# Performance work log

Measured on AMD Instinct MI355X. Metric: run time of the kernel, lower is better.

The kernel has to match this reference:

```python
import jax, jax.numpy as jnp
import numpy as np

DIM = 512
HEADS = 8
LANDMARKS = 64


def setup_inputs() -> dict:
    key = jax.random.key(0)
    ks = jax.random.split(key, 9)
    B, N, C = 2, 16384, DIM
    s = 0.02
    return {
        "x": jax.random.normal(ks[0], (B, N, C), dtype=jnp.float32),
        "wq": jax.random.normal(ks[1], (C, C), dtype=jnp.float32) * s,
        "bq": jnp.zeros((C,), dtype=jnp.float32),
        "wk": jax.random.normal(ks[2], (C, C), dtype=jnp.float32) * s,
        "bk": jnp.zeros((C,), dtype=jnp.float32),
        "wv": jax.random.normal(ks[3], (C, C), dtype=jnp.float32) * s,
        "bv": jnp.zeros((C,), dtype=jnp.float32),
        "wo": jax.random.normal(ks[4], (C, C), dtype=jnp.float32) * s,
        "bo": jnp.zeros((C,), dtype=jnp.float32),
    }


def _to_heads(x, H):
    B, N, C = x.shape
    return x.reshape(B, N, H, C // H).transpose(0, 2, 1, 3)  # (B,H,N,hd)


def reference(x, wq, bq, wk, bk, wv, bv, wo, bo):
    B, N, C = x.shape
    H = HEADS
    hd = C // H
    scale = hd ** (-0.5)
    m = min(LANDMARKS, N)

    q = _to_heads(x @ wq.T + bq, H) * scale  # (B,H,N,hd)
    k = _to_heads(x @ wk.T + bk, H)
    v = _to_heads(x @ wv.T + bv, H)

    if N <= m * 2:
        attn = jax.nn.softmax(jnp.einsum("bhnd,bhkd->bhnk", q, k), axis=-1)
        out = jnp.einsum("bhnk,bhkd->bhnd", attn, v)
    else:
        seg = (N + m - 1) // m
        pad = seg * m - N
        if pad > 0:
            q_p = jnp.pad(q, ((0, 0), (0, 0), (0, pad), (0, 0)))
            k_p = jnp.pad(k, ((0, 0), (0, 0), (0, pad), (0, 0)))
        else:
            q_p, k_p = q, k
        # landmarks: mean over consecutive segments of length seg (zero-pad included, as in torch)
        q_land = q_p.reshape(B, H, m, seg, hd).mean(3)  # (B,H,m,hd)
        k_land = k_p.reshape(B, H, m, seg, hd).mean(3)

        ker1 = jax.nn.softmax(jnp.einsum("bhnd,bhmd->bhnm", q, k_land), axis=-1)  # (B,H,N,m)
        ker2 = jax.nn.softmax(jnp.einsum("bhld,bhmd->bhlm", q_land, k_land), axis=-1)  # (B,H,m,m)
        ker3 = jax.nn.softmax(jnp.einsum("bhmd,bhnd->bhmn", q_land, k), axis=-1)  # (B,H,m,N)
        ker2_inv = jnp.linalg.pinv(ker2)  # (B,H,m,m)

        kv = jnp.einsum("bhmn,bhnd->bhmd", ker3, v)  # (B,H,m,hd)
        out = jnp.einsum("bhnm,bhmd->bhnd", ker1, ker2_inv @ kv)

    out = out.transpose(0, 2, 1, 3).reshape(B, N, C)
    return out @ wo.T + bo
```

## Files before the change

kernel.cpp:

```cpp
#include <hip/hip_runtime.h>
#include <stdint.h>


constexpr int B_   = 2;
constexpr int N_   = 16384;
constexpr int C_   = 512;
constexpr int H_   = 8;
constexpr int HD_  = 64;
constexpr int LM_  = 64;
constexpr int SEG_ = 256;
constexpr int BH_  = 16;
constexpr int NCH_ = 16;
constexpr int NPART_ = 64;
constexpr int SW1_ = 3;
constexpr int SW2_ = 2;

#define RCOND_ (640.0 * 1.1920928955078125e-07)

typedef unsigned short ushort4_t __attribute__((ext_vector_type(4)));
typedef unsigned short ushort8_t __attribute__((ext_vector_type(8)));
typedef __bf16 bf16x8 __attribute__((ext_vector_type(8)));
typedef float f32x4 __attribute__((ext_vector_type(4)));

__device__ inline float bf2f(unsigned short u) {
  union { unsigned int i; float f; } x; x.i = ((unsigned int)u) << 16; return x.f;
}
__device__ inline unsigned short f2bf(float f) {
  union { float f; unsigned int i; } x; x.f = f;
  unsigned int lsb = (x.i >> 16) & 1;
  return (unsigned short)((x.i + 0x7fffu + lsb) >> 16);
}
__device__ inline bf16x8 ld_bf8(const unsigned short* p) { return *(const bf16x8*)p; }

__device__ __forceinline__ void gload_lds16(const unsigned short* gsrc, unsigned short* ldst) {
  __builtin_amdgcn_global_load_lds((const __attribute__((address_space(1))) void*)gsrc,
                                   (__attribute__((address_space(3))) void*)ldst, 16, 0, 0);
}

__global__ __launch_bounds__(256) void cvt_w4_kernel(const float* __restrict__ wq,
                                                     const float* __restrict__ wk,
                                                     const float* __restrict__ wv,
                                                     const float* __restrict__ wo,
                                                     unsigned short* __restrict__ dq,
                                                     unsigned short* __restrict__ dk,
                                                     unsigned short* __restrict__ dv,
                                                     unsigned short* __restrict__ dwo) {
  int which = blockIdx.y;
  const float* src = which == 0 ? wq : which == 1 ? wk : which == 2 ? wv : wo;
  unsigned short* dst = which == 0 ? dq : which == 1 ? dk : which == 2 ? dv : dwo;
  int i = blockIdx.x * 256 + threadIdx.x;
  const float* s = src + (size_t)i * 8;
  float4 x0 = *(const float4*)(s);
  float4 x1 = *(const float4*)(s + 4);
  ushort8_t u;
  u[0] = f2bf(x0.x); u[1] = f2bf(x0.y); u[2] = f2bf(x0.z); u[3] = f2bf(x0.w);
  u[4] = f2bf(x1.x); u[5] = f2bf(x1.y); u[6] = f2bf(x1.z); u[7] = f2bf(x1.w);
  *(ushort8_t*)(dst + (size_t)i * 8) = u;
}

__global__ __launch_bounds__(256) void seg_mean_kernel(const float* __restrict__ x,
                                                       float* __restrict__ xbar,
                                                       unsigned short* __restrict__ xb) {
  int bl = blockIdx.x;
  int b = bl / LM_, l = bl % LM_;
  int t = threadIdx.x;
  int c4 = t & 127;
  int rh = t >> 7;
  const size_t rowbase = (size_t)b * N_ + (size_t)l * SEG_;
  const float* xp = x + rowbase * C_;
  float4 s = make_float4(0.f, 0.f, 0.f, 0.f);
  for (int r = rh * 128; r < rh * 128 + 128; ++r) {
    float4 v = *(const float4*)(xp + (size_t)r * C_ + c4 * 4);
    s.x += v.x; s.y += v.y; s.z += v.z; s.w += v.w;
    ushort4_t u;
    u[0] = f2bf(v.x); u[1] = f2bf(v.y); u[2] = f2bf(v.z); u[3] = f2bf(v.w);
    *(ushort4_t*)(xb + (rowbase + r) * C_ + c4 * 4) = u;
  }
  __shared__ float red[2][512];
  *(float4*)&red[rh][c4 * 4] = s;
  __syncthreads();
  if (rh == 0) {
    float4 a = *(float4*)&red[0][c4 * 4];
    float4 c = *(float4*)&red[1][c4 * 4];
    const float invs = 1.0f / SEG_;
    float4 o;
    o.x = (a.x + c.x) * invs; o.y = (a.y + c.y) * invs;
    o.z = (a.z + c.z) * invs; o.w = (a.w + c.w) * invs;
    *(float4*)(xbar + (size_t)bl * C_ + c4 * 4) = o;
  }
}

__global__ __launch_bounds__(256) void land_gemm_kernel(const float* __restrict__ xbar,
                                                        const float* __restrict__ wq,
                                                        const float* __restrict__ bq,
                                                        const float* __restrict__ wk,
                                                        const float* __restrict__ bk,
                                                        float* __restrict__ qland,
                                                        float* __restrict__ kland,
                                                        unsigned short* __restrict__ qlbh,
                                                        unsigned short* __restrict__ qlbl,
                                                        unsigned short* __restrict__ klb) {
  __shared__ float As[32][68];
  __shared__ float Ws[32][68];
  int which = blockIdx.x >> 1;
  int row0 = (blockIdx.x & 1) * 64;
  int col0 = blockIdx.y * 64;
  const float* A = xbar;
  const float* W = which ? wk : wq;
  const float* bias = which ? bk : bq;
  float scale = which ? 1.0f : 0.125f;
  float* out = which ? kland : qland;
  int tid = threadIdx.x;
  int tm = tid >> 4, tn = tid & 15;
  float acc[4][4] = {};
  for (int k0 = 0; k0 < C_; k0 += 32) {
#pragma unroll
    for (int i = 0; i < 2; ++i) {
      int s = tid + i * 256;
      int r = s >> 3;
      int kg = (s & 7) << 2;
      float4 av = *(const float4*)(A + (size_t)(row0 + r) * C_ + k0 + kg);
      As[kg + 0][r] = av.x; As[kg + 1][r] = av.y;
      As[kg + 2][r] = av.z; As[kg + 3][r] = av.w;
      float4 wv = *(const float4*)(W + (size_t)(col0 + r) * C_ + k0 + kg);
      Ws[kg + 0][r] = wv.x; Ws[kg + 1][r] = wv.y;
      Ws[kg + 2][r] = wv.z; Ws[kg + 3][r] = wv.w;
    }
    __syncthreads();
#pragma unroll
    for (int kk = 0; kk < 32; ++kk) {
      float4 a = *(const float4*)&As[kk][tm * 4];
      float4 b = *(const float4*)&Ws[kk][tn * 4];
      float av[4] = {a.x, a.y, a.z, a.w};
      float bv[4] = {b.x, b.y, b.z, b.w};
#pragma unroll
      for (int i = 0; i < 4; ++i)
#pragma unroll
        for (int j = 0; j < 4; ++j) acc[i][j] += av[i] * bv[j];
    }
    __syncthreads();
  }
#pragma unroll
  for (int i = 0; i < 4; ++i) {
    int row = row0 + tm * 4 + i;
    int d0 = tn * 4;
    float o4[4];
#pragma unroll
    for (int j = 0; j < 4; ++j) o4[j] = (acc[i][j] + bias[col0 + d0 + j]) * scale;
    int b = row / LM_, n = row % LM_;
    int h = col0 >> 6;
    size_t idx = (((size_t)(b * H_ + h) * LM_) + n) * HD_ + d0;
    float4 o; o.x = o4[0]; o.y = o4[1]; o.z = o4[2]; o.w = o4[3];
    *(float4*)(out + idx) = o;
    if (which == 0) {
      ushort4_t uh, ul;
#pragma unroll
      for (int j = 0; j < 4; ++j) {
        unsigned short hbits = f2bf(o4[j]);
        uh[j] = hbits;
        ul[j] = f2bf(o4[j] - bf2f(hbits));
      }
      *(ushort4_t*)(qlbh + idx) = uh;
      *(ushort4_t*)(qlbl + idx) = ul;
    } else {
      ushort4_t uk;
#pragma unroll
      for (int j = 0; j < 4; ++j) uk[j] = f2bf(o4[j]);
      *(ushort4_t*)(klb + idx) = uk;
    }
  }
}

__device__ __forceinline__ void dma_gemm_body(const unsigned short* __restrict__ A,
                                              const unsigned short* __restrict__ W,
                                              const float* __restrict__ bias,
                                              void* __restrict__ out,
                                              float scale, int omode,
                                              int row0, int col0,
                                              unsigned short* Xs, unsigned short* Wl,
                                              int tid) {
  int w = tid >> 6, lane = tid & 63;
  int wr = w >> 1, wc = w & 1;
  f32x4 acc[4][4] = {};

  for (int k0 = 0; k0 < C_; k0 += 32) {
    __syncthreads();
#pragma unroll
    for (int i = 0; i < 2; ++i) {
      const unsigned short* gx = A + (size_t)(row0 + w * 32 + i * 16 + (lane >> 2)) * C_ + k0 + (lane & 3) * 8;
      gload_lds16(gx, &Xs[(w * 32 + i * 16) * 32]);
      const unsigned short* gw = W + (size_t)(col0 + w * 32 + i * 16 + (lane >> 2)) * C_ + k0 + (lane & 3) * 8;
      gload_lds16(gw, &Wl[(w * 32 + i * 16) * 32]);
    }
    __syncthreads();
    bf16x8 af[4], bfr[4];
#pragma unroll
    for (int m = 0; m < 4; ++m)
      af[m] = *(bf16x8*)&Xs[(wr * 64 + m * 16 + (lane & 15)) * 32 + (lane >> 4) * 8];
#pragma unroll
    for (int n = 0; n < 4; ++n)
      bfr[n] = *(bf16x8*)&Wl[(wc * 64 + n * 16 + (lane & 15)) * 32 + (lane >> 4) * 8];
#pragma unroll
    for (int m = 0; m < 4; ++m)
#pragma unroll
      for (int n = 0; n < 4; ++n)
        acc[m][n] = __builtin_amdgcn_mfma_f32_16x16x32_bf16(af[m], bfr[n], acc[m][n], 0, 0, 0);
  }

#pragma unroll
  for (int m = 0; m < 4; ++m) {
    int rbase = row0 + wr * 64 + m * 16 + (lane >> 4) * 4;
#pragma unroll
    for (int n = 0; n < 4; ++n) {
      int c = col0 + wc * 64 + n * 16 + (lane & 15);
      float bc = bias[c];
      if (omode == 0) {
#pragma unroll
        for (int rg = 0; rg < 4; ++rg)
          ((float*)out)[(size_t)(rbase + rg) * C_ + c] = acc[m][n][rg] + bc;
      } else if (omode == 2) {
        int b = rbase >> 14, nn = rbase & 16383;
        int h = c >> 6, d = c & 63;
        ushort4_t u;
#pragma unroll
        for (int rg = 0; rg < 4; ++rg) u[rg] = f2bf((acc[m][n][rg] + bc) * scale);
        *(ushort4_t*)((unsigned short*)out + ((size_t)(b * H_ + h) * HD_ + d) * N_ + nn) = u;
      } else {
#pragma unroll
        for (int rg = 0; rg < 4; ++rg) {
          float val = (acc[m][n][rg] + bc) * scale;
          int r = rbase + rg;
          int b = r >> 14, nn = r & 16383, h = c >> 6, d = c & 63;
          ((unsigned short*)out)[(((size_t)(b * H_ + h) * N_) + nn) * HD_ + d] = f2bf(val);
        }
      }
    }
  }
}

__device__ __forceinline__ void svd_sweeps(float a[16], float v[16], char* smemraw,
                                           int w, int lane, int nsweeps) {
  float (*Ac)[68]    = (float(*)[68])(smemraw);
  float (*Vc)[68]    = (float(*)[68])(smemraw + 17408);
  float (*pg)[4][64] = (float(*)[4][64])(smemraw + 34816);
  float (*pa4)[64]   = (float(*)[64])(smemraw + 36864);
  const int r0 = w * 16;
  *(float4*)&Ac[lane][r0 + 0]  = make_float4(a[0], a[1], a[2], a[3]);
  *(float4*)&Ac[lane][r0 + 4]  = make_float4(a[4], a[5], a[6], a[7]);
  *(float4*)&Ac[lane][r0 + 8]  = make_float4(a[8], a[9], a[10], a[11]);
  *(float4*)&Ac[lane][r0 + 12] = make_float4(a[12], a[13], a[14], a[15]);
  *(float4*)&Vc[lane][r0 + 0]  = make_float4(v[0], v[1], v[2], v[3]);
  *(float4*)&Vc[lane][r0 + 4]  = make_float4(v[4], v[5], v[6], v[7]);
  *(float4*)&Vc[lane][r0 + 8]  = make_float4(v[8], v[9], v[10], v[11]);
  *(float4*)&Vc[lane][r0 + 12] = make_float4(v[12], v[13], v[14], v[15]);

  for (int sweep = 0; sweep < nsweeps; ++sweep) {
    float p0 = 0.f, p1 = 0.f;
#pragma unroll
    for (int k = 0; k < 16; k += 2) { p0 = fmaf(a[k], a[k], p0); p1 = fmaf(a[k + 1], a[k + 1], p1); }
    pa4[w][lane] = p0 + p1;
    __syncthreads();
    float alpha = (pa4[0][lane] + pa4[1][lane]) + (pa4[2][lane] + pa4[3][lane]);
    for (int mask = 1; mask < 64; ++mask) {
      int buf = mask & 1;
      int partner = lane ^ mask;
      bool lower = lane < partner;
      float beta = __shfl_xor(alpha, mask);
      float4 o0 = *(float4*)&Ac[partner][r0 + 0];
      float4 o1 = *(float4*)&Ac[partner][r0 + 4];
      float4 o2 = *(float4*)&Ac[partner][r0 + 8];
      float4 o3 = *(float4*)&Ac[partner][r0 + 12];
      float o[16] = {o0.x, o0.y, o0.z, o0.w, o1.x, o1.y, o1.z, o1.w,
                     o2.x, o2.y, o2.z, o2.w, o3.x, o3.y, o3.z, o3.w};
      float g0 = 0.f, g1 = 0.f;
#pragma unroll
      for (int k = 0; k < 16; k += 2) { g0 = fmaf(a[k], o[k], g0); g1 = fmaf(a[k + 1], o[k + 1], g1); }
      pg[buf][w][lane] = g0 + g1;
      __syncthreads();
      float gamma = (pg[buf][0][lane] + pg[buf][1][lane]) + (pg[buf][2][lane] + pg[buf][3][lane]);
      bool need = (gamma * gamma > 1e-12f * alpha * beta);
      if (__any(need)) {
        float4 q0 = *(float4*)&Vc[partner][r0 + 0];
        float4 q1 = *(float4*)&Vc[partner][r0 + 4];
        float4 q2 = *(float4*)&Vc[partner][r0 + 8];
        float4 q3 = *(float4*)&Vc[partner][r0 + 12];
        float ov[16] = {q0.x, q0.y, q0.z, q0.w, q1.x, q1.y, q1.z, q1.w,
                        q2.x, q2.y, q2.z, q2.w, q3.x, q3.y, q3.z, q3.w};
        float ap = lower ? alpha : beta;
        float aq = lower ? beta : alpha;
        float c = 1.f, s = 0.f;
        if (need) {
          float tau = (aq - ap) / (2.f * gamma);
          float t = copysignf(1.f, tau) / (fabsf(tau) + sqrtf(fmaf(tau, tau, 1.f)));
          c = rsqrtf(fmaf(t, t, 1.f));
          s = t * c;
        }
        float sm = lower ? -s : s;
#pragma unroll
        for (int k = 0; k < 16; ++k) a[k] = fmaf(sm, o[k], c * a[k]);
#pragma unroll
        for (int k = 0; k < 16; ++k) v[k] = fmaf(sm, ov[k], c * v[k]);
        float twocsg = 2.f * c * s * gamma;
        alpha = fmaf(c * c, alpha, fmaf(s * s, beta, lower ? -twocsg : twocsg));
        *(float4*)&Ac[lane][r0 + 0]  = make_float4(a[0], a[1], a[2], a[3]);
        *(float4*)&Ac[lane][r0 + 4]  = make_float4(a[4], a[5], a[6], a[7]);
        *(float4*)&Ac[lane][r0 + 8]  = make_float4(a[8], a[9], a[10], a[11]);
        *(float4*)&Ac[lane][r0 + 12] = make_float4(a[12], a[13], a[14], a[15]);
        *(float4*)&Vc[lane][r0 + 0]  = make_float4(v[0], v[1], v[2], v[3]);
        *(float4*)&Vc[lane][r0 + 4]  = make_float4(v[4], v[5], v[6], v[7]);
        *(float4*)&Vc[lane][r0 + 8]  = make_float4(v[8], v[9], v[10], v[11]);
        *(float4*)&Vc[lane][r0 + 12] = make_float4(v[12], v[13], v[14], v[15]);
      }
    }
  }
}

__device__ void svd_phase1(const float* __restrict__ qland, const float* __restrict__ kland,
                           float* __restrict__ asave, float* __restrict__ vsave,
                           int bh, char* smemraw, int tid) {
  __builtin_amdgcn_s_setprio(3);
  float (*qlS)[65] = (float(*)[65])(smemraw);
  float (*klS)[65] = (float(*)[65])(smemraw + 16640);
  for (int i = 0; i < 4; ++i) {
    int s = tid + i * 256;
    int r = s >> 4, d4 = (s & 15) << 2;
    *(float4*)&qlS[r][d4] = *(const float4*)(qland + ((size_t)bh * 64 + r) * 64 + d4);
    *(float4*)&klS[r][d4] = *(const float4*)(kland + ((size_t)bh * 64 + r) * 64 + d4);
  }
  __syncthreads();
  int w = tid >> 6, lane = tid & 63;
  float a[16], v[16];
#pragma unroll
  for (int k = 0; k < 16; ++k) {
    int row = w * 16 + k;
    float acc = 0.f;
#pragma unroll
    for (int d4 = 0; d4 < 64; d4 += 4) {
      float4 qv = *(float4*)&qlS[row][d4];
      float4 kv = *(float4*)&klS[lane][d4];
      acc += qv.x * kv.x + qv.y * kv.y + qv.z * kv.z + qv.w * kv.w;
    }
    float e = expf(acc);
    float rs = e;
#pragma unroll
    for (int m = 1; m < 64; m <<= 1) rs += __shfl_xor(rs, m);
    a[k] = e * (1.f / rs);
  }
#pragma unroll
  for (int k = 0; k < 16; ++k) v[k] = (w * 16 + k == lane) ? 1.f : 0.f;
  __syncthreads();
  svd_sweeps(a, v, smemraw, w, lane, SW1_);
#pragma unroll
  for (int k = 0; k < 16; ++k) {
    asave[((size_t)bh * 64 + w * 16 + k) * 64 + lane] = a[k];
    vsave[((size_t)bh * 64 + w * 16 + k) * 64 + lane] = v[k];
  }
  __builtin_amdgcn_s_setprio(0);
}

__device__ void svd_phase2(const float* __restrict__ asave, const float* __restrict__ vsave,
                           float* __restrict__ pinv, int bh, char* smemraw, int tid) {
  __builtin_amdgcn_s_setprio(3);
  double (*ps2)[64]  = (double(*)[64])(smemraw + 37888);
  float (*vsL)[65]   = (float(*)[65])(smemraw);
  float (*wasL)[65]  = (float(*)[65])(smemraw + 16640);
  int w = tid >> 6, lane = tid & 63;
  float a[16], v[16];
#pragma unroll
  for (int k = 0; k < 16; ++k) {
    a[k] = asave[((size_t)bh * 64 + w * 16 + k) * 64 + lane];
    v[k] = vsave[((size_t)bh * 64 + w * 16 + k) * 64 + lane];
  }
  svd_sweeps(a, v, smemraw, w, lane, SW2_);

  double psig = 0.0;
#pragma unroll
  for (int k = 0; k < 16; ++k) psig += (double)a[k] * (double)a[k];
  ps2[w][lane] = psig;
  __syncthreads();
  double sig2 = (ps2[0][lane] + ps2[1][lane]) + (ps2[2][lane] + ps2[3][lane]);
  double smax = sig2;
#pragma unroll
  for (int m = 1; m < 64; m <<= 1) smax = fmax(smax, __shfl_xor(smax, m));
  double cutoff2 = smax * (RCOND_ * RCOND_);
  float wgt = (sig2 > cutoff2) ? (float)(1.0 / sig2) : 0.f;

#pragma unroll
  for (int k = 0; k < 16; ++k) {
    vsL[lane][w * 16 + k] = v[k];
    wasL[lane][w * 16 + k] = wgt * a[k];
  }
  __syncthreads();
  int i = tid >> 2;
  int j0 = (tid & 3) * 16;
  float acc[16] = {};
  for (int r = 0; r < 64; ++r) {
    float vv = vsL[r][i];
#pragma unroll
    for (int jj = 0; jj < 16; ++jj) acc[jj] = fmaf(vv, wasL[r][j0 + jj], acc[jj]);
  }
#pragma unroll
  for (int jj = 0; jj < 16; jj += 4) {
    float4 ovv = make_float4(acc[jj], acc[jj + 1], acc[jj + 2], acc[jj + 3]);
    *(float4*)(pinv + ((size_t)bh * 64 + i) * 64 + j0 + jj) = ovv;
  }
  __builtin_amdgcn_s_setprio(0);
}

__global__ __launch_bounds__(256) void fused1_kernel(
    const unsigned short* __restrict__ xb,
    const unsigned short* __restrict__ wqb, const float* __restrict__ bq,
    const unsigned short* __restrict__ wkb, const float* __restrict__ bk,
    const unsigned short* __restrict__ wvb, const float* __restrict__ bv,
    unsigned short* __restrict__ q4, unsigned short* __restrict__ k4,
    unsigned short* __restrict__ vt,
    const float* __restrict__ qland, const float* __restrict__ kland,
    float* __restrict__ asave, float* __restrict__ vsave) {
  __shared__ __align__(16) char smem[37888];
  int tid = threadIdx.x;
  int blk = blockIdx.x;
  if (blk < 16) { svd_phase1(qland, kland, asave, vsave, blk, smem, tid); return; }
  int g = blk - 16;
  int which = g >> 10;
  int sub = g & 1023;
  int row0 = (sub >> 2) * 128;
  int col0 = (sub & 3) * 128;
  unsigned short* Xs = (unsigned short*)smem;
  unsigned short* Wl = Xs + 128 * 32;
  if (which == 0)
    dma_gemm_body(xb, wqb, bq, q4, 0.125f, 1, row0, col0, Xs, Wl, tid);
  else if (which == 1)
    dma_gemm_body(xb, wkb, bk, k4, 1.0f, 1, row0, col0, Xs, Wl, tid);
  else
    dma_gemm_body(xb, wvb, bv, vt, 1.0f, 2, row0, col0, Xs, Wl, tid);
}

__device__ void ker3kv_body(const unsigned short* __restrict__ qlh,
                            const unsigned short* __restrict__ qll,
                            const unsigned short* __restrict__ k4,
                            const unsigned short* __restrict__ vt,
                            float* __restrict__ pacc,
                            float* __restrict__ pacc0,
                            float* __restrict__ ps,
                            int bh, int ch, char* smemraw, int tid) {
  int w = tid >> 6, lane = tid & 63;
  int part = ch * 4 + w;
  int lrow = lane & 15, lgrp = lane >> 4;
  unsigned short* myP = (unsigned short*)smemraw + w * 64 * 72;

  bf16x8 qah[4][2], qal[4][2];
#pragma unroll
  for (int mf = 0; mf < 4; ++mf)
#pragma unroll
    for (int ks = 0; ks < 2; ++ks) {
      size_t off = ((size_t)bh * 64 + mf * 16 + lrow) * 64 + ks * 32 + lgrp * 8;
      qah[mf][ks] = ld_bf8(qlh + off);
      qal[mf][ks] = ld_bf8(qll + off);
    }
  bf16x8 onesf;
#pragma unroll
  for (int j = 0; j < 8; ++j) onesf[j] = (__bf16)1.0f;

  f32x4 kvacc[4][4] = {};
  f32x4 oneacc[4] = {};
  f32x4 ssum[4] = {};

  for (int sub = 0; sub < 4; ++sub) {
    int n0 = ch * 1024 + w * 256 + sub * 64;
    f32x4 sacc[4][4] = {};
#pragma unroll
    for (int ks = 0; ks < 2; ++ks) {
#pragma unroll
      for (int nf = 0; nf < 4; ++nf) {
        bf16x8 kb = ld_bf8(k4 + ((size_t)bh * N_ + n0 + nf * 16 + lrow) * 64 + ks * 32 + lgrp * 8);
#pragma unroll
        for (int mf = 0; mf < 4; ++mf) {
          sacc[mf][nf] = __builtin_amdgcn_mfma_f32_16x16x32_bf16(qah[mf][ks], kb, sacc[mf][nf], 0, 0, 0);
          sacc[mf][nf] = __builtin_amdgcn_mfma_f32_16x16x32_bf16(qal[mf][ks], kb, sacc[mf][nf], 0, 0, 0);
        }
      }
    }
#pragma unroll
    for (int mf = 0; mf < 4; ++mf) {
#pragma unroll
      for (int nf = 0; nf < 4; ++nf) {
#pragma unroll
        for (int r = 0; r < 4; ++r) {
          float pd = expf(sacc[mf][nf][r]) - 1.0f;
          ssum[mf][r] += pd;
          myP[(mf * 16 + lgrp * 4 + r) * 72 + nf * 16 + lrow] = f2bf(pd);
        }
      }
    }
#pragma unroll
    for (int ks = 0; ks < 2; ++ks) {
      bf16x8 pa[4];
#pragma unroll
      for (int mf = 0; mf < 4; ++mf)
        pa[mf] = ld_bf8(myP + (mf * 16 + lrow) * 72 + ks * 32 + lgrp * 8);
#pragma unroll
      for (int nf = 0; nf < 4; ++nf) {
        bf16x8 vb = ld_bf8(vt + ((size_t)bh * 64 + nf * 16 + lrow) * N_ + n0 + ks * 32 + lgrp * 8);
#pragma unroll
        for (int mf = 0; mf < 4; ++mf)
          kvacc[mf][nf] = __builtin_amdgcn_mfma_f32_16x16x32_bf16(pa[mf], vb, kvacc[mf][nf], 0, 0, 0);
        oneacc[nf] = __builtin_amdgcn_mfma_f32_16x16x32_bf16(onesf, vb, oneacc[nf], 0, 0, 0);
      }
    }
  }
#pragma unroll
  for (int mf = 0; mf < 4; ++mf)
#pragma unroll
    for (int m = 1; m < 16; m <<= 1)
#pragma unroll
      for (int r = 0; r < 4; ++r) ssum[mf][r] += __shfl_xor(ssum[mf][r], m);

  size_t pb = (((size_t)bh * NPART_ + part) * 64) * 64;
#pragma unroll
  for (int mf = 0; mf < 4; ++mf)
#pragma unroll
    for (int nf = 0; nf < 4; ++nf)
#pragma unroll
      for (int r = 0; r < 4; ++r)
        pacc[pb + (size_t)(mf * 16 + lgrp * 4 + r) * 64 + nf * 16 + lrow] = kvacc[mf][nf][r];
  if (lrow == 0) {
#pragma unroll
    for (int mf = 0; mf < 4; ++mf)
#pragma unroll
      for (int r = 0; r < 4; ++r)
        ps[((size_t)bh * NPART_ + part) * 64 + mf * 16 + lgrp * 4 + r] = ssum[mf][r];
  }
  if (lgrp == 0) {
#pragma unroll
    for (int nf = 0; nf < 4; ++nf)
      pacc0[((size_t)bh * NPART_ + part) * 64 + nf * 16 + lrow] = oneacc[nf][0];
  }
}

__global__ __launch_bounds__(256, 1) void fused2_kernel(
    const unsigned short* __restrict__ qlh,
    const unsigned short* __restrict__ qll,
    const unsigned short* __restrict__ k4,
    const unsigned short* __restrict__ vt,
    float* __restrict__ pacc, float* __restrict__ pacc0, float* __restrict__ ps,
    const float* __restrict__ asave, const float* __restrict__ vsave,
    float* __restrict__ pinv) {
  __shared__ __align__(16) char smem[39936];
  int tid = threadIdx.x;
  int blk = blockIdx.x;
  if (blk < 16) { svd_phase2(asave, vsave, pinv, blk, smem, tid); return; }
  int g = blk - 16;
  int bh = g >> 4, ch = g & 15;
  ker3kv_body(qlh, qll, k4, vt, pacc, pacc0, ps, bh, ch, smem, tid);
}

__global__ __launch_bounds__(256) void kv_combine_kernel(const float* __restrict__ pacc,
                                                         const float* __restrict__ pacc0,
                                                         const float* __restrict__ ps,
                                                         float* __restrict__ kv) {
  int bh = blockIdx.y;
  int lm = blockIdx.x * 16 + (threadIdx.x >> 4);
  int d4 = (threadIdx.x & 15) * 4;
  float s = 16384.f;
  for (int part = 0; part < NPART_; ++part) s += ps[((size_t)bh * NPART_ + part) * 64 + lm];
  float4 a = make_float4(0.f, 0.f, 0.f, 0.f);
  for (int part = 0; part < NPART_; ++part) {
    float4 c0 = *(const float4*)&pacc0[((size_t)bh * NPART_ + part) * 64 + d4];
    float4 v = *(const float4*)&pacc[(((size_t)bh * NPART_ + part) * 64 + lm) * 64 + d4];
    a.x += c0.x + v.x; a.y += c0.y + v.y; a.z += c0.z + v.z; a.w += c0.w + v.w;
  }
  float inv = 1.f / s;
  float4 o = make_float4(a.x * inv, a.y * inv, a.z * inv, a.w * inv);
  *(float4*)(kv + ((size_t)bh * 64 + lm) * 64 + d4) = o;
}

__global__ __launch_bounds__(256) void mmat_kernel(const float* __restrict__ pinv,
                                                   const float* __restrict__ kv,
                                                   unsigned short* __restrict__ mtbh,
                                                   unsigned short* __restrict__ mtbl,
                                                   float* __restrict__ msum) {
  int bh = blockIdx.x;
  int tid = threadIdx.x;
  __shared__ float kvs[64][68];
  __shared__ double pcsd[64];
  for (int i = 0; i < 4; ++i) {
    int s = tid + i * 256;
    int r = s >> 4, d4 = (s & 15) << 2;
    *(float4*)&kvs[r][d4] = *(const float4*)(kv + ((size_t)bh * 64 + r) * 64 + d4);
  }
  if (tid < 64) {
    double s = 0.0;
    for (int l = 0; l < 64; ++l) s += (double)pinv[((size_t)bh * 64 + l) * 64 + tid];
    pcsd[tid] = s;
  }
  __syncthreads();
  int l = tid >> 2, t = tid & 3;
  double o[16] = {};
  for (int j = 0; j < 64; ++j) {
    double pv = (double)pinv[((size_t)bh * 64 + l) * 64 + j];
#pragma unroll
    for (int i = 0; i < 16; ++i) o[i] += pv * (double)kvs[j][t * 16 + i];
  }
#pragma unroll
  for (int i = 0; i < 16; ++i) {
    float f = (float)o[i];
    unsigned short hi = f2bf(f);
    float lo = f - bf2f(hi);
    int d = t * 16 + i;
    mtbh[((size_t)bh * 64 + d) * 64 + l] = hi;
    mtbl[((size_t)bh * 64 + d) * 64 + l] = f2bf(lo);
  }
  if (tid < 64) {
    double m = 0.0;
    for (int j = 0; j < 64; ++j) m += pcsd[j] * (double)kvs[j][tid];
    msum[(size_t)bh * 64 + tid] = (float)(m * (1.0 / 64.0));
  }
}

__global__ __launch_bounds__(256, 1) void ker1out_mfma_kernel(
    const unsigned short* __restrict__ q4,
    const unsigned short* __restrict__ klb,
    const unsigned short* __restrict__ mtbh,
    const unsigned short* __restrict__ mtbl,
    const float* __restrict__ msum,
    unsigned short* __restrict__ outh) {
  int bh = blockIdx.y, tile = blockIdx.x;
  int b = bh >> 3, h = bh & 7;
  int tid = threadIdx.x, w = tid >> 6, lane = tid & 63;
  int lrow = lane & 15, lgrp = lane >> 4;
  int tok0 = tile * 256 + w * 64;
  __shared__ __align__(16) unsigned short Pl[4][64 * 72];
  unsigned short* myP = &Pl[w][0];

  f32x4 sacc[4][4] = {};
#pragma unroll
  for (int ks = 0; ks < 2; ++ks) {
    bf16x8 kb[4];
#pragma unroll
    for (int nf = 0; nf < 4; ++nf)
      kb[nf] = ld_bf8(klb + ((size_t)bh * 64 + nf * 16 + lrow) * 64 + ks * 32 + lgrp * 8);
#pragma unroll
    for (int mf = 0; mf < 4; ++mf) {
      bf16x8 qa = ld_bf8(q4 + ((size_t)bh * N_ + tok0 + mf * 16 + lrow) * 64 + ks * 32 + lgrp * 8);
#pragma unroll
      for (int nf = 0; nf < 4; ++nf)
        sacc[mf][nf] = __builtin_amdgcn_mfma_f32_16x16x32_bf16(qa, kb[nf], sacc[mf][nf], 0, 0, 0);
    }
  }
  f32x4 ssum[4] = {};
#pragma unroll
  for (int mf = 0; mf < 4; ++mf)
#pragma unroll
    for (int nf = 0; nf < 4; ++nf)
#pragma unroll
      for (int r = 0; r < 4; ++r) {
        sacc[mf][nf][r] = expf(sacc[mf][nf][r]);
        ssum[mf][r] += sacc[mf][nf][r];
      }
#pragma unroll
  for (int mf = 0; mf < 4; ++mf)
#pragma unroll
    for (int m = 1; m < 16; m <<= 1)
#pragma unroll
      for (int r = 0; r < 4; ++r) ssum[mf][r] += __shfl_xor(ssum[mf][r], m);
#pragma unroll
  for (int mf = 0; mf < 4; ++mf) {
    f32x4 inv;
#pragma unroll
    for (int r = 0; r < 4; ++r) inv[r] = 1.f / ssum[mf][r];
#pragma unroll
    for (int nf = 0; nf < 4; ++nf)
#pragma unroll
      for (int r = 0; r < 4; ++r) {
        float pdev = fmaf(sacc[mf][nf][r], inv[r], -0.015625f);
        myP[(mf * 16 + lgrp * 4 + r) * 72 + nf * 16 + lrow] = f2bf(pdev);
      }
  }

  f32x4 oacc[4][4] = {};
#pragma unroll
  for (int ks = 0; ks < 2; ++ks) {
    bf16x8 pa[4];
#pragma unroll
    for (int mf = 0; mf < 4; ++mf)
      pa[mf] = ld_bf8(myP + (mf * 16 + lrow) * 72 + ks * 32 + lgrp * 8);
#pragma unroll
    for (int nf = 0; nf < 4; ++nf) {
      bf16x8 mh = ld_bf8(mtbh + ((size_t)bh * 64 + nf * 16 + lrow) * 64 + ks * 32 + lgrp * 8);
      bf16x8 ml = ld_bf8(mtbl + ((size_t)bh * 64 + nf * 16 + lrow) * 64 + ks * 32 + lgrp * 8);
#pragma unroll
      for (int mf = 0; mf < 4; ++mf) {
        oacc[mf][nf] = __builtin_amdgcn_mfma_f32_16x16x32_bf16(pa[mf], mh, oacc[mf][nf], 0, 0, 0);
        oacc[mf][nf] = __builtin_amdgcn_mfma_f32_16x16x32_bf16(pa[mf], ml, oacc[mf][nf], 0, 0, 0);
      }
    }
  }
#pragma unroll
  for (int nf = 0; nf < 4; ++nf) {
    float ms = msum[(size_t)bh * 64 + nf * 16 + lrow];
#pragma unroll
    for (int mf = 0; mf < 4; ++mf)
#pragma unroll
      for (int r = 0; r < 4; ++r) {
        int tok = tok0 + mf * 16 + lgrp * 4 + r;
        int d = nf * 16 + lrow;
        outh[((size_t)b * N_ + tok) * C_ + h * HD_ + d] = f2bf(oacc[mf][nf][r] + ms);
      }
  }
}

__global__ __launch_bounds__(256) void oproj_kernel(const unsigned short* __restrict__ outh,
                                                    const unsigned short* __restrict__ wob,
                                                    const float* __restrict__ bo,
                                                    float* __restrict__ out) {
  __shared__ __align__(16) unsigned short Xs[128 * 32];
  __shared__ __align__(16) unsigned short Wl[128 * 32];
  dma_gemm_body(outh, wob, bo, out, 1.0f, 0, blockIdx.x * 128, blockIdx.y * 128,
                Xs, Wl, threadIdx.x);
}

extern "C" void kernel_launch(void* const* d_in, const int* in_sizes, int n_in,
                              void* d_out, int out_size, void* d_ws, size_t ws_size,
                              hipStream_t stream) {
  const float* x  = (const float*)d_in[0];
  const float* wq = (const float*)d_in[1];
  const float* bq = (const float*)d_in[2];
  const float* wk = (const float*)d_in[3];
  const float* bk = (const float*)d_in[4];
  const float* wv = (const float*)d_in[5];
  const float* bv = (const float*)d_in[6];
  const float* wo = (const float*)d_in[7];
  const float* bo = (const float*)d_in[8];
  float* out = (float*)d_out;

  char* base = (char*)d_ws;
  const size_t QKV = (size_t)BH_ * N_ * HD_;
  unsigned short* q4 = (unsigned short*)base;
  unsigned short* k4 = (unsigned short*)(base + QKV * 2);
  unsigned short* vt = (unsigned short*)(base + QKV * 4);
  unsigned short* outh = (unsigned short*)(base + QKV * 2);
  char* sp = base + QKV * 6;
  float* pacc  = (float*)sp; sp += (size_t)BH_ * NPART_ * 64 * 64 * 4;
  float* pacc0 = (float*)sp; sp += (size_t)BH_ * NPART_ * 64 * 4;
  float* ps    = (float*)sp; sp += (size_t)BH_ * NPART_ * 64 * 4;
  float* xbar  = (float*)sp; sp += (size_t)B_ * LM_ * C_ * 4;
  float* qland = (float*)sp; sp += (size_t)BH_ * LM_ * HD_ * 4;
  float* kland = (float*)sp; sp += (size_t)BH_ * LM_ * HD_ * 4;
  unsigned short* qlbh = (unsigned short*)sp; sp += (size_t)BH_ * LM_ * HD_ * 2;
  unsigned short* qlbl = (unsigned short*)sp; sp += (size_t)BH_ * LM_ * HD_ * 2;
  unsigned short* klb  = (unsigned short*)sp; sp += (size_t)BH_ * LM_ * HD_ * 2;
  float* pinv  = (float*)sp; sp += (size_t)BH_ * LM_ * LM_ * 4;
  float* kvb   = (float*)sp; sp += (size_t)BH_ * LM_ * HD_ * 4;
  unsigned short* mtbh = (unsigned short*)sp; sp += (size_t)BH_ * LM_ * HD_ * 2;
  unsigned short* mtbl = (unsigned short*)sp; sp += (size_t)BH_ * LM_ * HD_ * 2;
  float* msum  = (float*)sp; sp += (size_t)BH_ * HD_ * 4;
  float* asave = (float*)sp; sp += (size_t)BH_ * LM_ * LM_ * 4;
  float* vsave = (float*)sp; sp += (size_t)BH_ * LM_ * LM_ * 4;
  unsigned short* wob = (unsigned short*)sp; sp += (size_t)C_ * C_ * 2;
  unsigned short* wqb = (unsigned short*)sp; sp += (size_t)C_ * C_ * 2;
  unsigned short* wkb = (unsigned short*)sp; sp += (size_t)C_ * C_ * 2;
  unsigned short* wvb = (unsigned short*)sp; sp += (size_t)C_ * C_ * 2;

  unsigned short* xb = (unsigned short*)d_out;

  const int W8 = (C_ * C_) / 8;

  dim3 gc(W8 / 256, 4);
  cvt_w4_kernel<<<gc, 256, 0, stream>>>(wq, wk, wv, wo, wqb, wkb, wvb, wob);

  seg_mean_kernel<<<B_ * LM_, 256, 0, stream>>>(x, xbar, xb);
  dim3 gl(4, 8);
  land_gemm_kernel<<<gl, 256, 0, stream>>>(xbar, wq, bq, wk, bk,
                                           qland, kland, qlbh, qlbl, klb);

  fused1_kernel<<<16 + 3 * 1024, 256, 0, stream>>>(
      xb, wqb, bq, wkb, bk, wvb, bv, q4, k4, vt, qland, kland, asave, vsave);

  fused2_kernel<<<16 + NCH_ * BH_, 256, 0, stream>>>(
      qlbh, qlbl, k4, vt, pacc, pacc0, ps, asave, vsave, pinv);

  dim3 g7(4, BH_);
  kv_combine_kernel<<<g7, 256, 0, stream>>>(pacc, pacc0, ps, kvb);
  mmat_kernel<<<BH_, 256, 0, stream>>>(pinv, kvb, mtbh, mtbl, msum);

  dim3 g9(N_ / 256, BH_);
  ker1out_mfma_kernel<<<g9, 256, 0, stream>>>(q4, klb, mtbh, mtbl, msum, outh);

  dim3 g10(B_ * N_ / 128, C_ / 128);
  oproj_kernel<<<g10, 256, 0, stream>>>(outh, wob, bo, out);
}
```

Baseline: 447.2 us.

## Widen fused1 blocks to 512 threads, pairing GEMM tiles and splitting SVD over 8 waves

The fused QKV-projection plus SVD kernel now launches 512-thread blocks. Each GEMM block packs two independent 128x128 tiles in separate LDS halves, and the SVD phase-1 blocks spread the 64 Jacobi rows across 8 waves of 8 rows instead of 4 waves of 16. The SVD sweep routine is templated on the wave count. The goal is to shorten the serial critical path of the SVD blocks, which otherwise run alongside the GEMM work, and to cut the block count. The cost is more frequent barriers per Jacobi rotation across 8 waves, and possibly lower occupancy or scheduling flexibility for the paired GEMM tiles.

```diff
diff --git a/kernel.cpp b/kernel.cpp
--- a/kernel.cpp
+++ b/kernel.cpp
@@ -238,54 +238,63 @@
   }
 }
 
-__device__ __forceinline__ void svd_sweeps(float a[16], float v[16], char* smemraw,
+template <int NW>
+__device__ __forceinline__ void svd_sweeps(float* a, float* v, char* smemraw,
                                            int w, int lane, int nsweeps) {
-  float (*Ac)[68]    = (float(*)[68])(smemraw);
-  float (*Vc)[68]    = (float(*)[68])(smemraw + 17408);
-  float (*pg)[4][64] = (float(*)[4][64])(smemraw + 34816);
-  float (*pa4)[64]   = (float(*)[64])(smemraw + 36864);
-  const int r0 = w * 16;
-  *(float4*)&Ac[lane][r0 + 0]  = make_float4(a[0], a[1], a[2], a[3]);
-  *(float4*)&Ac[lane][r0 + 4]  = make_float4(a[4], a[5], a[6], a[7]);
-  *(float4*)&Ac[lane][r0 + 8]  = make_float4(a[8], a[9], a[10], a[11]);
-  *(float4*)&Ac[lane][r0 + 12] = make_float4(a[12], a[13], a[14], a[15]);
-  *(float4*)&Vc[lane][r0 + 0]  = make_float4(v[0], v[1], v[2], v[3]);
-  *(float4*)&Vc[lane][r0 + 4]  = make_float4(v[4], v[5], v[6], v[7]);
-  *(float4*)&Vc[lane][r0 + 8]  = make_float4(v[8], v[9], v[10], v[11]);
-  *(float4*)&Vc[lane][r0 + 12] = make_float4(v[12], v[13], v[14], v[15]);
+  constexpr int RP = 64 / NW;
+  float (*Ac)[68] = (float(*)[68])(smemraw);
+  float (*Vc)[68] = (float(*)[68])(smemraw + 17408);
+  float (*pg)[NW][64] = (float(*)[NW][64])(smemraw + 34816);
+  float (*pa)[64] = (float(*)[64])(smemraw + 34816 + 2 * NW * 64 * 4);
+  const int r0 = w * RP;
+#pragma unroll
+  for (int c = 0; c < RP; c += 4) {
+    *(float4*)&Ac[lane][r0 + c] = make_float4(a[c], a[c + 1], a[c + 2], a[c + 3]);
+    *(float4*)&Vc[lane][r0 + c] = make_float4(v[c], v[c + 1], v[c + 2], v[c + 3]);
+  }
 
   for (int sweep = 0; sweep < nsweeps; ++sweep) {
     float p0 = 0.f, p1 = 0.f;
 #pragma unroll
-    for (int k = 0; k < 16; k += 2) { p0 = fmaf(a[k], a[k], p0); p1 = fmaf(a[k + 1], a[k + 1], p1); }
-    pa4[w][lane] = p0 + p1;
+    for (int k = 0; k < RP; k += 2) { p0 = fmaf(a[k], a[k], p0); p1 = fmaf(a[k + 1], a[k + 1], p1); }
+    pa[w][lane] = p0 + p1;
     __syncthreads();
-    float alpha = (pa4[0][lane] + pa4[1][lane]) + (pa4[2][lane] + pa4[3][lane]);
+    float alpha;
+    if constexpr (NW == 4)
+      alpha = (pa[0][lane] + pa[1][lane]) + (pa[2][lane] + pa[3][lane]);
+    else
+      alpha = ((pa[0][lane] + pa[1][lane]) + (pa[2][lane] + pa[3][lane])) +
+              ((pa[4][lane] + pa[5][lane]) + (pa[6][lane] + pa[7][lane]));
     for (int mask = 1; mask < 64; ++mask) {
       int buf = mask & 1;
       int partner = lane ^ mask;
       bool lower = lane < partner;
       float beta = __shfl_xor(alpha, mask);
-      float4 o0 = *(float4*)&Ac[partner][r0 + 0];
-      float4 o1 = *(float4*)&Ac[partner][r0 + 4];
-      float4 o2 = *(float4*)&Ac[partner][r0 + 8];
-      float4 o3 = *(float4*)&Ac[partner][r0 + 12];
-      float o[16] = {o0.x, o0.y, o0.z, o0.w, o1.x, o1.y, o1.z, o1.w,
-                     o2.x, o2.y, o2.z, o2.w, o3.x, o3.y, o3.z, o3.w};
+      float o[RP];
+#pragma unroll
+      for (int c = 0; c < RP; c += 4) {
+        float4 t4 = *(float4*)&Ac[partner][r0 + c];
+        o[c] = t4.x; o[c + 1] = t4.y; o[c + 2] = t4.z; o[c + 3] = t4.w;
+      }
       float g0 = 0.f, g1 = 0.f;
 #pragma unroll
-      for (int k = 0; k < 16; k += 2) { g0 = fmaf(a[k], o[k], g0); g1 = fmaf(a[k + 1], o[k + 1], g1); }
+      for (int k = 0; k < RP; k += 2) { g0 = fmaf(a[k], o[k], g0); g1 = fmaf(a[k + 1], o[k + 1], g1); }
       pg[buf][w][lane] = g0 + g1;
       __syncthreads();
-      float gamma = (pg[buf][0][lane] + pg[buf][1][lane]) + (pg[buf][2][lane] + pg[buf][3][lane]);
+      float gamma;
+      if constexpr (NW == 4)
+        gamma = (pg[buf][0][lane] + pg[buf][1][lane]) + (pg[buf][2][lane] + pg[buf][3][lane]);
+      else
+        gamma = ((pg[buf][0][lane] + pg[buf][1][lane]) + (pg[buf][2][lane] + pg[buf][3][lane])) +
+                ((pg[buf][4][lane] + pg[buf][5][lane]) + (pg[buf][6][lane] + pg[buf][7][lane]));
       bool need = (gamma * gamma > 1e-12f * alpha * beta);
       if (__any(need)) {
-        float4 q0 = *(float4*)&Vc[partner][r0 + 0];
-        float4 q1 = *(float4*)&Vc[partner][r0 + 4];
-        float4 q2 = *(float4*)&Vc[partner][r0 + 8];
-        float4 q3 = *(float4*)&Vc[partner][r0 + 12];
-        float ov[16] = {q0.x, q0.y, q0.z, q0.w, q1.x, q1.y, q1.z, q1.w,
-                        q2.x, q2.y, q2.z, q2.w, q3.x, q3.y, q3.z, q3.w};
+        float ov[RP];
+#pragma unroll
+        for (int c = 0; c < RP; c += 4) {
+          float4 t4 = *(float4*)&Vc[partner][r0 + c];
+          ov[c] = t4.x; ov[c + 1] = t4.y; ov[c + 2] = t4.z; ov[c + 3] = t4.w;
+        }
         float ap = lower ? alpha : beta;
         float aq = lower ? beta : alpha;
         float c = 1.f, s = 0.f;
@@ -297,19 +306,16 @@
         }
         float sm = lower ? -s : s;
 #pragma unroll
-        for (int k = 0; k < 16; ++k) a[k] = fmaf(sm, o[k], c * a[k]);
-#pragma unroll
-        for (int k = 0; k < 16; ++k) v[k] = fmaf(sm, ov[k], c * v[k]);
+        for (int k = 0; k < RP; ++k) a[k] = fmaf(sm, o[k], c * a[k]);
+#pragma unroll
+        for (int k = 0; k < RP; ++k) v[k] = fmaf(sm, ov[k], c * v[k]);
         float twocsg = 2.f * c * s * gamma;
         alpha = fmaf(c * c, alpha, fmaf(s * s, beta, lower ? -twocsg : twocsg));
-        *(float4*)&Ac[lane][r0 + 0]  = make_float4(a[0], a[1], a[2], a[3]);
-        *(float4*)&Ac[lane][r0 + 4]  = make_float4(a[4], a[5], a[6], a[7]);
-        *(float4*)&Ac[lane][r0 + 8]  = make_float4(a[8], a[9], a[10], a[11]);
-        *(float4*)&Ac[lane][r0 + 12] = make_float4(a[12], a[13], a[14], a[15]);
-        *(float4*)&Vc[lane][r0 + 0]  = make_float4(v[0], v[1], v[2], v[3]);
-        *(float4*)&Vc[lane][r0 + 4]  = make_float4(v[4], v[5], v[6], v[7]);
-        *(float4*)&Vc[lane][r0 + 8]  = make_float4(v[8], v[9], v[10], v[11]);
-        *(float4*)&Vc[lane][r0 + 12] = make_float4(v[12], v[13], v[14], v[15]);
+#pragma unroll
+        for (int cc = 0; cc < RP; cc += 4) {
+          *(float4*)&Ac[lane][r0 + cc] = make_float4(a[cc], a[cc + 1], a[cc + 2], a[cc + 3]);
+          *(float4*)&Vc[lane][r0 + cc] = make_float4(v[cc], v[cc + 1], v[cc + 2], v[cc + 3]);
+        }
       }
     }
   }
@@ -321,18 +327,18 @@
   __builtin_amdgcn_s_setprio(3);
   float (*qlS)[65] = (float(*)[65])(smemraw);
   float (*klS)[65] = (float(*)[65])(smemraw + 16640);
-  for (int i = 0; i < 4; ++i) {
-    int s = tid + i * 256;
+  for (int i = 0; i < 2; ++i) {
+    int s = tid + i * 512;
     int r = s >> 4, d4 = (s & 15) << 2;
     *(float4*)&qlS[r][d4] = *(const float4*)(qland + ((size_t)bh * 64 + r) * 64 + d4);
     *(float4*)&klS[r][d4] = *(const float4*)(kland + ((size_t)bh * 64 + r) * 64 + d4);
   }
   __syncthreads();
   int w = tid >> 6, lane = tid & 63;
-  float a[16], v[16];
-#pragma unroll
-  for (int k = 0; k < 16; ++k) {
-    int row = w * 16 + k;
+  float a[8], v[8];
+#pragma unroll
+  for (int k = 0; k < 8; ++k) {
+    int row = w * 8 + k;
     float acc = 0.f;
 #pragma unroll
     for (int d4 = 0; d4 < 64; d4 += 4) {
@@ -347,13 +353,13 @@
     a[k] = e * (1.f / rs);
   }
 #pragma unroll
-  for (int k = 0; k < 16; ++k) v[k] = (w * 16 + k == lane) ? 1.f : 0.f;
+  for (int k = 0; k < 8; ++k) v[k] = (w * 8 + k == lane) ? 1.f : 0.f;
   __syncthreads();
-  svd_sweeps(a, v, smemraw, w, lane, SW1_);
-#pragma unroll
-  for (int k = 0; k < 16; ++k) {
-    asave[((size_t)bh * 64 + w * 16 + k) * 64 + lane] = a[k];
-    vsave[((size_t)bh * 64 + w * 16 + k) * 64 + lane] = v[k];
+  svd_sweeps<8>(a, v, smemraw, w, lane, SW1_);
+#pragma unroll
+  for (int k = 0; k < 8; ++k) {
+    asave[((size_t)bh * 64 + w * 8 + k) * 64 + lane] = a[k];
+    vsave[((size_t)bh * 64 + w * 8 + k) * 64 + lane] = v[k];
   }
   __builtin_amdgcn_s_setprio(0);
 }
@@ -371,7 +377,7 @@
     a[k] = asave[((size_t)bh * 64 + w * 16 + k) * 64 + lane];
     v[k] = vsave[((size_t)bh * 64 + w * 16 + k) * 64 + lane];
   }
-  svd_sweeps(a, v, smemraw, w, lane, SW2_);
+  svd_sweeps<4>(a, v, smemraw, w, lane, SW2_);
 
   double psig = 0.0;
 #pragma unroll
@@ -407,7 +413,7 @@
   __builtin_amdgcn_s_setprio(0);
 }
 
-__global__ __launch_bounds__(256) void fused1_kernel(
+__global__ __launch_bounds__(512) void fused1_kernel(
     const unsigned short* __restrict__ xb,
     const unsigned short* __restrict__ wqb, const float* __restrict__ bq,
     const unsigned short* __restrict__ wkb, const float* __restrict__ bk,
@@ -416,23 +422,26 @@
     unsigned short* __restrict__ vt,
     const float* __restrict__ qland, const float* __restrict__ kland,
     float* __restrict__ asave, float* __restrict__ vsave) {
-  __shared__ __align__(16) char smem[37888];
+  __shared__ __align__(16) char smem[40960];
   int tid = threadIdx.x;
   int blk = blockIdx.x;
   if (blk < 16) { svd_phase1(qland, kland, asave, vsave, blk, smem, tid); return; }
   int g = blk - 16;
-  int which = g >> 10;
-  int sub = g & 1023;
+  int which = g >> 9;
+  int subpair = g & 511;
+  int half = tid >> 8;
+  int ltid = tid & 255;
+  int sub = subpair * 2 + half;
   int row0 = (sub >> 2) * 128;
   int col0 = (sub & 3) * 128;
-  unsigned short* Xs = (unsigned short*)smem;
+  unsigned short* Xs = (unsigned short*)(smem + half * 16384);
   unsigned short* Wl = Xs + 128 * 32;
   if (which == 0)
-    dma_gemm_body(xb, wqb, bq, q4, 0.125f, 1, row0, col0, Xs, Wl, tid);
+    dma_gemm_body(xb, wqb, bq, q4, 0.125f, 1, row0, col0, Xs, Wl, ltid);
   else if (which == 1)
-    dma_gemm_body(xb, wkb, bk, k4, 1.0f, 1, row0, col0, Xs, Wl, tid);
+    dma_gemm_body(xb, wkb, bk, k4, 1.0f, 1, row0, col0, Xs, Wl, ltid);
   else
-    dma_gemm_body(xb, wvb, bv, vt, 1.0f, 2, row0, col0, Xs, Wl, tid);
+    dma_gemm_body(xb, wvb, bv, vt, 1.0f, 2, row0, col0, Xs, Wl, ltid);
 }
 
 __device__ void ker3kv_body(const unsigned short* __restrict__ qlh,
@@ -773,7 +782,7 @@
   land_gemm_kernel<<<gl, 256, 0, stream>>>(xbar, wq, bq, wk, bk,
                                            qland, kland, qlbh, qlbl, klb);
 
-  fused1_kernel<<<16 + 3 * 1024, 256, 0, stream>>>(
+  fused1_kernel<<<16 + 3 * 512, 512, 0, stream>>>(
       xb, wqb, bq, wkb, bk, wvb, bv, q4, k4, vt, qland, kland, asave, vsave);
 
   fused2_kernel<<<16 + NCH_ * BH_, 256, 0, stream>>>(
```

After: 429.0 us. 1.04x faster.
